# Performance work log

Measured on AMD Instinct MI355X. Metric: run time of the kernel, lower is better.

Reference implementation:

```python
import jax, jax.numpy as jnp
import numpy as np

N = 50000      # nodes
E = 600000     # edges (avg degree 12)
IN = 128       # in_feat
HID = IN // 2  # 64
OUT = 128      # out_feat (must equal in_feat, see msg_linear)

# NOTE: the torch source uses nn.LeakyReLU(True): the positional arg is
# negative_slope, so slope == 1.0 (identity). We reproduce that faithfully.
NEG_SLOPE = 1.0

def leaky(v):
    return jnp.where(v >= 0, v, NEG_SLOPE * v)

def _linear_params(key, fan_in, fan_out):
    kw, kb = jax.random.split(key)
    bound = 1.0 / np.sqrt(fan_in)
    W = jax.random.uniform(kw, (fan_in, fan_out), jnp.float32, -bound, bound)
    b = jax.random.uniform(kb, (fan_out,), jnp.float32, -bound, bound)
    return W, b

def setup_inputs() -> dict:
    key = jax.random.key(0)
    ks = jax.random.split(key, 10)
    x = jax.random.normal(ks[0], (N, IN), jnp.float32)
    e = jax.random.normal(ks[1], (E, IN), jnp.float32)
    src = jax.random.randint(ks[2], (E,), 0, N, jnp.int64)
    dst = jax.random.randint(ks[3], (E,), 0, N, jnp.int64)
    W_nl1, b_nl1 = _linear_params(ks[4], IN, HID)    # node_linear1
    W_el, b_el = _linear_params(ks[5], IN, HID)      # edge_linear
    W1, b1 = _linear_params(ks[6], HID, HID)         # node_mlp layer 1
    W2, b2 = _linear_params(ks[7], HID, OUT)         # node_mlp layer 2
    W_nl2, b_nl2 = _linear_params(ks[8], IN, HID)    # node_linear2
    km, ke = jax.random.split(ks[9])
    W_ml, b_ml = _linear_params(km, IN, HID)         # msg_linear (in_feat==out_feat)
    W_em, b_em = _linear_params(ke, HID, OUT)        # edge_mlp layer
    return dict(x=x, e=e, src=src, dst=dst,
                W_nl1=W_nl1, b_nl1=b_nl1, W_el=W_el, b_el=b_el,
                W1=W1, b1=b1, W2=W2, b2=b2,
                W_nl2=W_nl2, b_nl2=b_nl2, W_ml=W_ml, b_ml=b_ml,
                W_em=W_em, b_em=b_em)

def reference(x, e, src, dst,
              W_nl1, b_nl1, W_el, b_el,
              W1, b1, W2, b2,
              W_nl2, b_nl2, W_ml, b_ml,
              W_em, b_em):
    # apply_edges: e' = node_mlp(node_linear1(x[src]) + edge_linear(e))
    z = x[src] @ W_nl1 + b_nl1 + e @ W_el + b_el            # [E, HID]
    e_new = leaky(leaky(z) @ W1 + b1) @ W2 + b2             # [E, OUT]
    # update_all(copy_e, sum): scatter-sum edge messages to destination nodes
    msg = jax.ops.segment_sum(e_new, dst, num_segments=N)   # [N, OUT]
    # x' = edge_mlp(node_linear2(x) + msg_linear(msg))
    h = leaky(x @ W_nl2 + b_nl2 + msg @ W_ml + b_ml)        # [N, HID]
    return h @ W_em + b_em                                  # [N, OUT]
```

## Files before the change

kernel.cpp:

```cpp
#include <hip/hip_runtime.h>

#define N_NODES 50000
#define N_EDGES 600000

#define WF_XS   0
#define WF_ES   6400000
#define WF_UN   12800000
#define WI_CNT   16000000
#define WI_OFF   16050000
#define WI_CUR   16100000
#define WI_BSUM  16150000
#define WI_BOFF  16150256
#define WI_EPAIR 16150512
#define WF_T2   17350528
#define WF_BEG  17354624
#define WF_RH   17354752
#define WF_K1   17354816
#define WF_WA   17358912
#define WF_R    17383488
#define WF_C2   17383616

#define NBLK_SCAN 196

__global__ __launch_bounds__(256) void pre_t2_kernel(
        const float* __restrict__ W2, const float* __restrict__ W_ml,
        const float* __restrict__ b1, const float* __restrict__ b2,
        float* __restrict__ T2, float* __restrict__ be_g) {
    int idx = blockIdx.x * 256 + threadIdx.x;
    if (idx < 4096) {
        int i = idx >> 6, j = idx & 63;
        float s = 0.f;
        for (int k = 0; k < 128; ++k) s += W2[i*128+k] * W_ml[k*64+j];
        T2[idx] = s;
    } else if (idx < 4224) {
        int j = idx - 4096;
        float s = b2[j];
        for (int k = 0; k < 64; ++k) s += b1[k] * W2[k*128+j];
        be_g[j] = s;
    }
}

__global__ __launch_bounds__(256) void pre_k1_kernel(
        const float* __restrict__ W1, const float* __restrict__ T2,
        float* __restrict__ K1) {
    int idx = blockIdx.x * 256 + threadIdx.x;
    if (idx >= 4096) return;
    int i = idx >> 6, j = idx & 63;
    float s = 0.f;
    for (int k = 0; k < 64; ++k) s += W1[i*64+k] * T2[k*64+j];
    K1[idx] = s;
}

__global__ __launch_bounds__(256) void pre_wa_kernel(
        const float* __restrict__ W_nl1, const float* __restrict__ W_el,
        const float* __restrict__ W_nl2, const float* __restrict__ K1,
        const float* __restrict__ b_nl1, const float* __restrict__ b_el,
        const float* __restrict__ be_g, const float* __restrict__ W_ml,
        float* __restrict__ WA, float* __restrict__ rh_g) {
    int idx = blockIdx.x * 256 + threadIdx.x;
    if (idx < 8192) {
        WA[idx] = W_nl2[idx];
    } else if (idx < 16384) {
        int p = idx - 8192; int i = p >> 6, j = p & 63;
        float s = 0.f;
        for (int k = 0; k < 64; ++k) s += W_nl1[i*64+k] * K1[k*64+j];
        WA[idx] = s;
    } else if (idx < 24576) {
        int p = idx - 16384; int i = p >> 6, j = p & 63;
        float s = 0.f;
        for (int k = 0; k < 64; ++k) s += W_el[i*64+k] * K1[k*64+j];
        WA[idx] = s;
    } else if (idx < 24640) {
        int t = idx - 24576;
        float s = 0.f;
        for (int k = 0; k < 64; ++k)  s += (b_nl1[k] + b_el[k]) * K1[k*64+t];
        for (int k = 0; k < 128; ++k) s += be_g[k] * W_ml[k*64+t];
        rh_g[t] = s;
    }
}

__global__ __launch_bounds__(256) void pre_rc_kernel(
        const float* __restrict__ rh_g, const float* __restrict__ W_em,
        const float* __restrict__ b_nl2, const float* __restrict__ b_ml,
        const float* __restrict__ b_em,
        float* __restrict__ r, float* __restrict__ c2) {
    int idx = threadIdx.x;
    if (idx < 128) {
        float s = 0.f;
        for (int k = 0; k < 64; ++k) s += rh_g[k] * W_em[k*128+idx];
        r[idx] = s;
    } else {
        int j = idx - 128;
        float s = b_em[j];
        for (int k = 0; k < 64; ++k) s += (b_nl2[k] + b_ml[k]) * W_em[k*128+j];
        c2[j] = s;
    }
}

__global__ __launch_bounds__(256) void zero_kernel(int* __restrict__ cnt) {
    int i = blockIdx.x * 256 + threadIdx.x;
    if (i < N_NODES) cnt[i] = 0;
}

__global__ __launch_bounds__(256) void hist_kernel(const int* __restrict__ dst,
                                                   int* __restrict__ cnt) {
    int e = blockIdx.x * 256 + threadIdx.x;
    if (e < N_EDGES) atomicAdd(&cnt[dst[e]], 1);
}

__global__ __launch_bounds__(256) void scan_a_kernel(const int* __restrict__ cnt,
                                                     int* __restrict__ bsum) {
    __shared__ int s[256];
    int i = blockIdx.x * 256 + threadIdx.x;
    int v = (i < N_NODES) ? cnt[i] : 0;
    s[threadIdx.x] = v;
    __syncthreads();
    for (int d = 128; d > 0; d >>= 1) {
        if (threadIdx.x < d) s[threadIdx.x] += s[threadIdx.x + d];
        __syncthreads();
    }
    if (threadIdx.x == 0) bsum[blockIdx.x] = s[0];
}

__global__ __launch_bounds__(256) void scan_b_kernel(const int* __restrict__ bsum,
                                                     int* __restrict__ boff) {
    __shared__ int s[256];
    int t = threadIdx.x;
    int v = (t < NBLK_SCAN) ? bsum[t] : 0;
    s[t] = v;
    __syncthreads();
    for (int d = 1; d < 256; d <<= 1) {
        int tv = (t >= d) ? s[t - d] : 0;
        __syncthreads();
        s[t] += tv;
        __syncthreads();
    }
    if (t < NBLK_SCAN) boff[t] = s[t] - v;
}

__global__ __launch_bounds__(256) void scan_c_kernel(const int* __restrict__ cnt,
                                                     const int* __restrict__ boff,
                                                     int* __restrict__ offs,
                                                     int* __restrict__ cursor) {
    __shared__ int s[256];
    int i = blockIdx.x * 256 + threadIdx.x;
    int t = threadIdx.x;
    int v = (i < N_NODES) ? cnt[i] : 0;
    s[t] = v;
    __syncthreads();
    for (int d = 1; d < 256; d <<= 1) {
        int tv = (t >= d) ? s[t - d] : 0;
        __syncthreads();
        s[t] += tv;
        __syncthreads();
    }
    if (i < N_NODES) {
        int ex = s[t] - v + boff[blockIdx.x];
        offs[i] = ex;
        cursor[i] = ex;
    }
}

__global__ __launch_bounds__(256) void fill_kernel(const int* __restrict__ dst,
                                                   const int* __restrict__ src,
                                                   int* __restrict__ cursor,
                                                   int2* __restrict__ epair) {
    int e = blockIdx.x * 256 + threadIdx.x;
    if (e < N_EDGES) {
        int pos = atomicAdd(&cursor[dst[e]], 1);
        epair[pos] = make_int2(e, src[e]);
    }
}

__global__ __launch_bounds__(256) void gather_kernel(
        const float* __restrict__ x, const float* __restrict__ ef,
        const int* __restrict__ cnt, const int* __restrict__ offs,
        const int2* __restrict__ epair,
        float* __restrict__ xs, float* __restrict__ es) {
    int n    = (int)((blockIdx.x * 256 + threadIdx.x) >> 6);
    int lane = threadIdx.x & 63;
    if (n >= N_NODES) return;
    int off = offs[n], deg = cnt[n];
    int col2 = lane * 2;
    float ax0 = 0.f, ax1 = 0.f, ae0 = 0.f, ae1 = 0.f;
    for (int c0 = 0; c0 < deg; c0 += 64) {
        int j = c0 + lane;
        int2 p = make_int2(0, 0);
        if (j < deg) p = epair[off + j];
        int m = deg - c0; if (m > 64) m = 64;
        int j2 = 0;
        for (; j2 + 8 <= m; j2 += 8) {
            float2 xv[8], ev[8];
            #pragma unroll
            for (int u = 0; u < 8; ++u) {
                int e_ = __shfl(p.x, j2 + u);
                int s_ = __shfl(p.y, j2 + u);
                xv[u] = *(const float2*)(x  + (size_t)s_ * 128 + col2);
                ev[u] = *(const float2*)(ef + (size_t)e_ * 128 + col2);
            }
            #pragma unroll
            for (int u = 0; u < 8; ++u) {
                ax0 += xv[u].x; ax1 += xv[u].y;
                ae0 += ev[u].x; ae1 += ev[u].y;
            }
        }
        for (; j2 < m; ++j2) {
            int e_ = __shfl(p.x, j2);
            int s_ = __shfl(p.y, j2);
            float2 xv = *(const float2*)(x  + (size_t)s_ * 128 + col2);
            float2 ev = *(const float2*)(ef + (size_t)e_ * 128 + col2);
            ax0 += xv.x; ax1 += xv.y;
            ae0 += ev.x; ae1 += ev.y;
        }
    }
    *(float2*)(xs + (size_t)n * 128 + col2) = make_float2(ax0, ax1);
    *(float2*)(es + (size_t)n * 128 + col2) = make_float2(ae0, ae1);
}

__global__ __launch_bounds__(256) void gemm1_kernel(
        const float* __restrict__ x, const float* __restrict__ xs,
        const float* __restrict__ es, const float* __restrict__ WA,
        float* __restrict__ u) {
    __shared__ float As[32][133];
    __shared__ float Ws[32][64];
    int base = blockIdx.x * 128;
    int t = threadIdx.x;
    int cg = t & 15, rg = t >> 4;
    int c0 = cg * 4, r0 = rg * 8;

    float acc[8][4];
    #pragma unroll
    for (int i = 0; i < 8; ++i)
        #pragma unroll
        for (int j = 0; j < 4; ++j) acc[i][j] = 0.f;

    int arow0 = t >> 3;
    int akq   = t & 7;

    #pragma unroll
    for (int m = 0; m < 3; ++m) {
        const float* __restrict__ S = (m == 0) ? x : (m == 1) ? xs : es;
        for (int k0 = 0; k0 < 128; k0 += 32) {
            __syncthreads();
            #pragma unroll
            for (int i = 0; i < 4; ++i) {
                int row = arow0 + i * 32;
                int n = base + row;
                float4 v = make_float4(0.f, 0.f, 0.f, 0.f);
                if (n < N_NODES)
                    v = *(const float4*)&S[(size_t)n * 128 + k0 + akq * 4];
                As[akq * 4 + 0][row] = v.x;
                As[akq * 4 + 1][row] = v.y;
                As[akq * 4 + 2][row] = v.z;
                As[akq * 4 + 3][row] = v.w;
            }
            #pragma unroll
            for (int i = 0; i < 2; ++i) {
                int idx = t + i * 256;
                int row = idx >> 4, q4 = idx & 15;
                *(float4*)&Ws[row][q4 * 4] =
                    *(const float4*)&WA[(size_t)(m * 128 + k0 + row) * 64 + q4 * 4];
            }
            __syncthreads();
            #pragma unroll 8
            for (int k = 0; k < 32; ++k) {
                float a[8];
                *(float4*)&a[0] = *(const float4*)&As[k][r0];
                *(float4*)&a[4] = *(const float4*)&As[k][r0 + 4];
                float4 w = *(const float4*)&Ws[k][c0];
                #pragma unroll
                for (int i = 0; i < 8; ++i) {
                    acc[i][0] += a[i] * w.x;
                    acc[i][1] += a[i] * w.y;
                    acc[i][2] += a[i] * w.z;
                    acc[i][3] += a[i] * w.w;
                }
            }
        }
    }

    #pragma unroll
    for (int i = 0; i < 8; ++i) {
        int n = base + r0 + i;
        if (n < N_NODES)
            *(float4*)&u[(size_t)n * 64 + c0] = *(float4*)&acc[i][0];
    }
}

__global__ __launch_bounds__(256) void gemm2_kernel(
        const float* __restrict__ u, const int* __restrict__ cnt,
        const float* __restrict__ W_em,
        const float* __restrict__ rvec, const float* __restrict__ c2,
        float* __restrict__ out) {
    __shared__ float UsT[64][69];
    __shared__ float Wem[64][128];
    int base = blockIdx.x * 64;
    int t = threadIdx.x;
    int cg = t & 15, rg = t >> 4;
    int c0 = cg * 8, r0 = rg * 4;

    #pragma unroll
    for (int i = 0; i < 4; ++i) {
        int idx = t + i * 256;
        int row = idx >> 4, kq = idx & 15;
        int n = base + row;
        float4 v = make_float4(0.f, 0.f, 0.f, 0.f);
        if (n < N_NODES) v = *(const float4*)&u[(size_t)n * 64 + kq * 4];
        UsT[kq * 4 + 0][row] = v.x;
        UsT[kq * 4 + 1][row] = v.y;
        UsT[kq * 4 + 2][row] = v.z;
        UsT[kq * 4 + 3][row] = v.w;
    }
    #pragma unroll
    for (int i = 0; i < 8; ++i) {
        int idx = t + i * 256;
        int row = idx >> 5, q4 = idx & 31;
        *(float4*)&Wem[row][q4 * 4] = *(const float4*)&W_em[(size_t)row * 128 + q4 * 4];
    }

    float4 rva = *(const float4*)&rvec[c0];
    float4 rvb = *(const float4*)&rvec[c0 + 4];
    float4 cva = *(const float4*)&c2[c0];
    float4 cvb = *(const float4*)&c2[c0 + 4];
    float acc[4][8];
    #pragma unroll
    for (int i = 0; i < 4; ++i) {
        int n = base + r0 + i;
        float dg = (n < N_NODES) ? (float)cnt[n] : 0.f;
        acc[i][0] = cva.x + dg * rva.x;  acc[i][1] = cva.y + dg * rva.y;
        acc[i][2] = cva.z + dg * rva.z;  acc[i][3] = cva.w + dg * rva.w;
        acc[i][4] = cvb.x + dg * rvb.x;  acc[i][5] = cvb.y + dg * rvb.y;
        acc[i][6] = cvb.z + dg * rvb.z;  acc[i][7] = cvb.w + dg * rvb.w;
    }
    __syncthreads();

    #pragma unroll 8
    for (int k = 0; k < 64; ++k) {
        float a[4], w[8];
        *(float4*)&a[0] = *(const float4*)&UsT[k][r0];
        *(float4*)&w[0] = *(const float4*)&Wem[k][c0];
        *(float4*)&w[4] = *(const float4*)&Wem[k][c0 + 4];
        #pragma unroll
        for (int i = 0; i < 4; ++i)
            #pragma unroll
            for (int j = 0; j < 8; ++j)
                acc[i][j] += a[i] * w[j];
    }

    #pragma unroll
    for (int i = 0; i < 4; ++i) {
        int n = base + r0 + i;
        if (n < N_NODES) {
            *(float4*)&out[(size_t)n * 128 + c0]     = *(float4*)&acc[i][0];
            *(float4*)&out[(size_t)n * 128 + c0 + 4] = *(float4*)&acc[i][4];
        }
    }
}

extern "C" void kernel_launch(void* const* d_in, const int* in_sizes, int n_in,
                              void* d_out, int out_size, void* d_ws, size_t ws_size,
                              hipStream_t stream) {
    const float* x     = (const float*)d_in[0];
    const float* ef    = (const float*)d_in[1];
    const int*   src   = (const int*)d_in[2];
    const int*   dst   = (const int*)d_in[3];
    const float* W_nl1 = (const float*)d_in[4];
    const float* b_nl1 = (const float*)d_in[5];
    const float* W_el  = (const float*)d_in[6];
    const float* b_el  = (const float*)d_in[7];
    const float* W1    = (const float*)d_in[8];
    const float* b1    = (const float*)d_in[9];
    const float* W2    = (const float*)d_in[10];
    const float* b2    = (const float*)d_in[11];
    const float* W_nl2 = (const float*)d_in[12];
    const float* b_nl2 = (const float*)d_in[13];
    const float* W_ml  = (const float*)d_in[14];
    const float* b_ml  = (const float*)d_in[15];
    const float* W_em  = (const float*)d_in[16];
    const float* b_em  = (const float*)d_in[17];

    int*   wsI = (int*)d_ws;
    float* wsF = (float*)d_ws;
    float* xs     = wsF + WF_XS;
    float* es     = wsF + WF_ES;
    float* uN     = wsF + WF_UN;
    int*   cnt    = wsI + WI_CNT;
    int*   offs   = wsI + WI_OFF;
    int*   cursor = wsI + WI_CUR;
    int*   bsum   = wsI + WI_BSUM;
    int*   boff   = wsI + WI_BOFF;
    int2*  epair  = (int2*)(wsI + WI_EPAIR);
    float* T2   = wsF + WF_T2;
    float* be_g = wsF + WF_BEG;
    float* rh_g = wsF + WF_RH;
    float* K1   = wsF + WF_K1;
    float* WA   = wsF + WF_WA;
    float* r    = wsF + WF_R;
    float* c2   = wsF + WF_C2;

    pre_t2_kernel<<<17, 256, 0, stream>>>(W2, W_ml, b1, b2, T2, be_g);
    pre_k1_kernel<<<16, 256, 0, stream>>>(W1, T2, K1);
    pre_wa_kernel<<<97, 256, 0, stream>>>(W_nl1, W_el, W_nl2, K1,
                                          b_nl1, b_el, be_g, W_ml, WA, rh_g);
    pre_rc_kernel<<<1, 256, 0, stream>>>(rh_g, W_em, b_nl2, b_ml, b_em, r, c2);

    zero_kernel<<<NBLK_SCAN, 256, 0, stream>>>(cnt);
    hist_kernel<<<(N_EDGES + 255) / 256, 256, 0, stream>>>(dst, cnt);
    scan_a_kernel<<<NBLK_SCAN, 256, 0, stream>>>(cnt, bsum);
    scan_b_kernel<<<1, 256, 0, stream>>>(bsum, boff);
    scan_c_kernel<<<NBLK_SCAN, 256, 0, stream>>>(cnt, boff, offs, cursor);
    fill_kernel<<<(N_EDGES + 255) / 256, 256, 0, stream>>>(dst, src, cursor, epair);

    gather_kernel<<<(N_NODES + 3) / 4, 256, 0, stream>>>(
        x, ef, cnt, offs, epair, xs, es);

    gemm1_kernel<<<(N_NODES + 127) / 128, 256, 0, stream>>>(x, xs, es, WA, uN);
    gemm2_kernel<<<(N_NODES + 63) / 64, 256, 0, stream>>>(
        uN, cnt, W_em, r, c2, (float*)d_out);
}
```

Measured before the change: 278.9 us.

## Project x to 64-dim before gathering to halve gathered node feature traffic

```diff
diff --git a/kernel.cpp b/kernel.cpp
--- a/kernel.cpp
+++ b/kernel.cpp
@@ -3,8 +3,11 @@
 #define N_NODES 50000
 #define N_EDGES 600000
 
-#define WF_XS   0
-#define WF_ES   6400000
+typedef float v2f __attribute__((ext_vector_type(2)));
+
+#define WF_PX   0
+#define WF_ES   3200000
+#define WF_PXS  9600000
 #define WF_UN   12800000
 #define WI_CNT   16000000
 #define WI_OFF   16050000
@@ -17,6 +20,7 @@
 #define WF_RH   17354752
 #define WF_K1   17354816
 #define WF_WA   17358912
+#define WF_WX1  17375296
 #define WF_R    17383488
 #define WF_C2   17383616
 
@@ -56,20 +60,21 @@
         const float* __restrict__ W_nl2, const float* __restrict__ K1,
         const float* __restrict__ b_nl1, const float* __restrict__ b_el,
         const float* __restrict__ be_g, const float* __restrict__ W_ml,
-        float* __restrict__ WA, float* __restrict__ rh_g) {
+        float* __restrict__ WA, float* __restrict__ WX1,
+        float* __restrict__ rh_g) {
     int idx = blockIdx.x * 256 + threadIdx.x;
     if (idx < 8192) {
         WA[idx] = W_nl2[idx];
     } else if (idx < 16384) {
         int p = idx - 8192; int i = p >> 6, j = p & 63;
         float s = 0.f;
-        for (int k = 0; k < 64; ++k) s += W_nl1[i*64+k] * K1[k*64+j];
+        for (int k = 0; k < 64; ++k) s += W_el[i*64+k] * K1[k*64+j];
         WA[idx] = s;
     } else if (idx < 24576) {
         int p = idx - 16384; int i = p >> 6, j = p & 63;
         float s = 0.f;
-        for (int k = 0; k < 64; ++k) s += W_el[i*64+k] * K1[k*64+j];
-        WA[idx] = s;
+        for (int k = 0; k < 64; ++k) s += W_nl1[i*64+k] * K1[k*64+j];
+        WX1[p] = s;
     } else if (idx < 24640) {
         int t = idx - 24576;
         float s = 0.f;
@@ -172,54 +177,115 @@
     }
 }
 
+__global__ __launch_bounds__(256) void px_kernel(
+        const float* __restrict__ x, const float* __restrict__ WX1,
+        float* __restrict__ px) {
+    __shared__ float As[32][133];
+    __shared__ float Ws[32][64];
+    int base = blockIdx.x * 128;
+    int t = threadIdx.x;
+    int cg = t & 15, rg = t >> 4;
+    int c0 = cg * 4, r0 = rg * 8;
+
+    float acc[8][4];
+    #pragma unroll
+    for (int i = 0; i < 8; ++i)
+        #pragma unroll
+        for (int j = 0; j < 4; ++j) acc[i][j] = 0.f;
+
+    int arow0 = t >> 3;
+    int akq   = t & 7;
+
+    for (int k0 = 0; k0 < 128; k0 += 32) {
+        __syncthreads();
+        #pragma unroll
+        for (int i = 0; i < 4; ++i) {
+            int row = arow0 + i * 32;
+            int n = base + row;
+            float4 v = make_float4(0.f, 0.f, 0.f, 0.f);
+            if (n < N_NODES)
+                v = *(const float4*)&x[(size_t)n * 128 + k0 + akq * 4];
+            As[akq * 4 + 0][row] = v.x;
+            As[akq * 4 + 1][row] = v.y;
+            As[akq * 4 + 2][row] = v.z;
+            As[akq * 4 + 3][row] = v.w;
+        }
+        #pragma unroll
+        for (int i = 0; i < 2; ++i) {
+            int idx = t + i * 256;
+            int row = idx >> 4, q4 = idx & 15;
+            *(float4*)&Ws[row][q4 * 4] =
+                *(const float4*)&WX1[(size_t)(k0 + row) * 64 + q4 * 4];
+        }
+        __syncthreads();
+        #pragma unroll 8
+        for (int k = 0; k < 32; ++k) {
+            float a[8];
+            *(float4*)&a[0] = *(const float4*)&As[k][r0];
+            *(float4*)&a[4] = *(const float4*)&As[k][r0 + 4];
+            float4 w = *(const float4*)&Ws[k][c0];
+            #pragma unroll
+            for (int i = 0; i < 8; ++i) {
+                acc[i][0] += a[i] * w.x;
+                acc[i][1] += a[i] * w.y;
+                acc[i][2] += a[i] * w.z;
+                acc[i][3] += a[i] * w.w;
+            }
+        }
+    }
+
+    #pragma unroll
+    for (int i = 0; i < 8; ++i) {
+        int n = base + r0 + i;
+        if (n < N_NODES)
+            *(float4*)&px[(size_t)n * 64 + c0] = *(float4*)&acc[i][0];
+    }
+}
+
 __global__ __launch_bounds__(256) void gather_kernel(
-        const float* __restrict__ x, const float* __restrict__ ef,
+        const float* __restrict__ px, const float* __restrict__ ef,
         const int* __restrict__ cnt, const int* __restrict__ offs,
         const int2* __restrict__ epair,
-        float* __restrict__ xs, float* __restrict__ es) {
+        float* __restrict__ pxs, float* __restrict__ es) {
     int n    = (int)((blockIdx.x * 256 + threadIdx.x) >> 6);
     int lane = threadIdx.x & 63;
     if (n >= N_NODES) return;
     int off = offs[n], deg = cnt[n];
     int col2 = lane * 2;
-    float ax0 = 0.f, ax1 = 0.f, ae0 = 0.f, ae1 = 0.f;
+    float apx = 0.f, ae0 = 0.f, ae1 = 0.f;
     for (int c0 = 0; c0 < deg; c0 += 64) {
         int j = c0 + lane;
         int2 p = make_int2(0, 0);
         if (j < deg) p = epair[off + j];
         int m = deg - c0; if (m > 64) m = 64;
-        int j2 = 0;
-        for (; j2 + 8 <= m; j2 += 8) {
-            float2 xv[8], ev[8];
+        for (int j2 = 0; j2 < m; j2 += 8) {
+            float xv[8]; v2f ev[8]; float msk[8];
             #pragma unroll
             for (int u = 0; u < 8; ++u) {
-                int e_ = __shfl(p.x, j2 + u);
-                int s_ = __shfl(p.y, j2 + u);
-                xv[u] = *(const float2*)(x  + (size_t)s_ * 128 + col2);
-                ev[u] = *(const float2*)(ef + (size_t)e_ * 128 + col2);
+                int jj = j2 + u;
+                int idx = (jj < m) ? jj : (m - 1);
+                msk[u] = (jj < m) ? 1.f : 0.f;
+                int e_ = __shfl(p.x, idx);
+                int s_ = __shfl(p.y, idx);
+                xv[u] = px[(size_t)s_ * 64 + lane];
+                ev[u] = __builtin_nontemporal_load(
+                            (const v2f*)(ef + (size_t)e_ * 128 + col2));
             }
             #pragma unroll
             for (int u = 0; u < 8; ++u) {
-                ax0 += xv[u].x; ax1 += xv[u].y;
-                ae0 += ev[u].x; ae1 += ev[u].y;
-            }
-        }
-        for (; j2 < m; ++j2) {
-            int e_ = __shfl(p.x, j2);
-            int s_ = __shfl(p.y, j2);
-            float2 xv = *(const float2*)(x  + (size_t)s_ * 128 + col2);
-            float2 ev = *(const float2*)(ef + (size_t)e_ * 128 + col2);
-            ax0 += xv.x; ax1 += xv.y;
-            ae0 += ev.x; ae1 += ev.y;
-        }
-    }
-    *(float2*)(xs + (size_t)n * 128 + col2) = make_float2(ax0, ax1);
+                apx += msk[u] * xv[u];
+                ae0 += msk[u] * ev[u][0];
+                ae1 += msk[u] * ev[u][1];
+            }
+        }
+    }
+    pxs[(size_t)n * 64 + lane] = apx;
     *(float2*)(es + (size_t)n * 128 + col2) = make_float2(ae0, ae1);
 }
 
 __global__ __launch_bounds__(256) void gemm1_kernel(
-        const float* __restrict__ x, const float* __restrict__ xs,
-        const float* __restrict__ es, const float* __restrict__ WA,
+        const float* __restrict__ x, const float* __restrict__ es,
+        const float* __restrict__ pxs, const float* __restrict__ WA,
         float* __restrict__ u) {
     __shared__ float As[32][133];
     __shared__ float Ws[32][64];
@@ -230,16 +296,19 @@
 
     float acc[8][4];
     #pragma unroll
-    for (int i = 0; i < 8; ++i)
-        #pragma unroll
-        for (int j = 0; j < 4; ++j) acc[i][j] = 0.f;
+    for (int i = 0; i < 8; ++i) {
+        int n = base + r0 + i;
+        float4 pv = make_float4(0.f, 0.f, 0.f, 0.f);
+        if (n < N_NODES) pv = *(const float4*)&pxs[(size_t)n * 64 + c0];
+        acc[i][0] = pv.x; acc[i][1] = pv.y; acc[i][2] = pv.z; acc[i][3] = pv.w;
+    }
 
     int arow0 = t >> 3;
     int akq   = t & 7;
 
     #pragma unroll
-    for (int m = 0; m < 3; ++m) {
-        const float* __restrict__ S = (m == 0) ? x : (m == 1) ? xs : es;
+    for (int m = 0; m < 2; ++m) {
+        const float* __restrict__ S = (m == 0) ? x : es;
         for (int k0 = 0; k0 < 128; k0 += 32) {
             __syncthreads();
             #pragma unroll
@@ -381,8 +450,9 @@
 
     int*   wsI = (int*)d_ws;
     float* wsF = (float*)d_ws;
-    float* xs     = wsF + WF_XS;
+    float* px     = wsF + WF_PX;
     float* es     = wsF + WF_ES;
+    float* pxs    = wsF + WF_PXS;
     float* uN     = wsF + WF_UN;
     int*   cnt    = wsI + WI_CNT;
     int*   offs   = wsI + WI_OFF;
@@ -395,13 +465,14 @@
     float* rh_g = wsF + WF_RH;
     float* K1   = wsF + WF_K1;
     float* WA   = wsF + WF_WA;
+    float* WX1  = wsF + WF_WX1;
     float* r    = wsF + WF_R;
     float* c2   = wsF + WF_C2;
 
     pre_t2_kernel<<<17, 256, 0, stream>>>(W2, W_ml, b1, b2, T2, be_g);
     pre_k1_kernel<<<16, 256, 0, stream>>>(W1, T2, K1);
     pre_wa_kernel<<<97, 256, 0, stream>>>(W_nl1, W_el, W_nl2, K1,
-                                          b_nl1, b_el, be_g, W_ml, WA, rh_g);
+                                          b_nl1, b_el, be_g, W_ml, WA, WX1, rh_g);
     pre_rc_kernel<<<1, 256, 0, stream>>>(rh_g, W_em, b_nl2, b_ml, b_em, r, c2);
 
     zero_kernel<<<NBLK_SCAN, 256, 0, stream>>>(cnt);
@@ -411,10 +482,12 @@
     scan_c_kernel<<<NBLK_SCAN, 256, 0, stream>>>(cnt, boff, offs, cursor);
     fill_kernel<<<(N_EDGES + 255) / 256, 256, 0, stream>>>(dst, src, cursor, epair);
 
+    px_kernel<<<(N_NODES + 127) / 128, 256, 0, stream>>>(x, WX1, px);
+
     gather_kernel<<<(N_NODES + 3) / 4, 256, 0, stream>>>(
-        x, ef, cnt, offs, epair, xs, es);
-
-    gemm1_kernel<<<(N_NODES + 127) / 128, 256, 0, stream>>>(x, xs, es, WA, uN);
+        px, ef, cnt, offs, epair, pxs, es);
+
+    gemm1_kernel<<<(N_NODES + 127) / 128, 256, 0, stream>>>(x, es, pxs, WA, uN);
     gemm2_kernel<<<(N_NODES + 63) / 64, 256, 0, stream>>>(
         uN, cnt, W_em, r, c2, (float*)d_out);
 }
```

Measured after the change: 252.2 us. -9.6%, faster.

## Precompute node projections before gather and fuse small setup kernels

Applied to the files above, without the earlier changes.

```diff
diff --git a/kernel.cpp b/kernel.cpp
--- a/kernel.cpp
+++ b/kernel.cpp
@@ -3,139 +3,152 @@
 #define N_NODES 50000
 #define N_EDGES 600000
 
-#define WF_XS   0
-#define WF_ES   6400000
-#define WF_UN   12800000
-#define WI_CNT   16000000
-#define WI_OFF   16050000
-#define WI_CUR   16100000
-#define WI_BSUM  16150000
-#define WI_BOFF  16150256
-#define WI_EPAIR 16150512
-#define WF_T2   17350528
-#define WF_BEG  17354624
-#define WF_RH   17354752
-#define WF_K1   17354816
-#define WF_WA   17358912
-#define WF_R    17383488
-#define WF_C2   17383616
+typedef float v2f __attribute__((ext_vector_type(2)));
+
+#define WF_PA   0
+#define WF_UN   6400000
+#define WI_CNT   9600000
+#define WI_OFF   9650000
+#define WI_CUR   9700000
+#define WI_BSUM  9750000
+#define WI_BOFF  9750256
+#define WI_EPAIR 9750512
+#define WF_T2   10950528
+#define WF_BEG  10954624
+#define WF_RH   10954752
+#define WF_K1   10954816
+#define WF_WAX  10958912
+#define WF_WE   10975296
+#define WF_R    10983488
+#define WF_C2   10983616
 
 #define NBLK_SCAN 196
-
-__global__ __launch_bounds__(256) void pre_t2_kernel(
+#define NBLK_E    2344
+#define NBLK_PT2  17
+#define NBLK_K1   16
+#define NBLK_WA   97
+#define NBLK_PXA  391
+
+__global__ __launch_bounds__(256) void f1_pret2_zero(
         const float* __restrict__ W2, const float* __restrict__ W_ml,
         const float* __restrict__ b1, const float* __restrict__ b2,
-        float* __restrict__ T2, float* __restrict__ be_g) {
-    int idx = blockIdx.x * 256 + threadIdx.x;
-    if (idx < 4096) {
+        float* __restrict__ T2, float* __restrict__ be_g,
+        int* __restrict__ cnt) {
+    int bid = blockIdx.x;
+    if (bid < NBLK_PT2) {
+        int idx = bid * 256 + threadIdx.x;
+        if (idx < 4096) {
+            int i = idx >> 6, j = idx & 63;
+            float s = 0.f;
+            for (int k = 0; k < 128; ++k) s += W2[i*128+k] * W_ml[k*64+j];
+            T2[idx] = s;
+        } else if (idx < 4224) {
+            int j = idx - 4096;
+            float s = b2[j];
+            for (int k = 0; k < 64; ++k) s += b1[k] * W2[k*128+j];
+            be_g[j] = s;
+        }
+    } else {
+        int i = (bid - NBLK_PT2) * 256 + threadIdx.x;
+        if (i < N_NODES) cnt[i] = 0;
+    }
+}
+
+__global__ __launch_bounds__(256) void f2_prek1_hist(
+        const float* __restrict__ W1, const float* __restrict__ T2,
+        float* __restrict__ K1,
+        const int* __restrict__ dst, int* __restrict__ cnt) {
+    int bid = blockIdx.x;
+    if (bid < NBLK_K1) {
+        int idx = bid * 256 + threadIdx.x;
         int i = idx >> 6, j = idx & 63;
         float s = 0.f;
-        for (int k = 0; k < 128; ++k) s += W2[i*128+k] * W_ml[k*64+j];
-        T2[idx] = s;
-    } else if (idx < 4224) {
-        int j = idx - 4096;
-        float s = b2[j];
-        for (int k = 0; k < 64; ++k) s += b1[k] * W2[k*128+j];
-        be_g[j] = s;
-    }
-}
-
-__global__ __launch_bounds__(256) void pre_k1_kernel(
-        const float* __restrict__ W1, const float* __restrict__ T2,
-        float* __restrict__ K1) {
-    int idx = blockIdx.x * 256 + threadIdx.x;
-    if (idx >= 4096) return;
-    int i = idx >> 6, j = idx & 63;
-    float s = 0.f;
-    for (int k = 0; k < 64; ++k) s += W1[i*64+k] * T2[k*64+j];
-    K1[idx] = s;
-}
-
-__global__ __launch_bounds__(256) void pre_wa_kernel(
+        for (int k = 0; k < 64; ++k) s += W1[i*64+k] * T2[k*64+j];
+        K1[idx] = s;
+    } else {
+        int e = (bid - NBLK_K1) * 256 + threadIdx.x;
+        if (e < N_EDGES) atomicAdd(&cnt[dst[e]], 1);
+    }
+}
+
+__global__ __launch_bounds__(256) void f3_prewa_scana(
         const float* __restrict__ W_nl1, const float* __restrict__ W_el,
         const float* __restrict__ W_nl2, const float* __restrict__ K1,
         const float* __restrict__ b_nl1, const float* __restrict__ b_el,
         const float* __restrict__ be_g, const float* __restrict__ W_ml,
-        float* __restrict__ WA, float* __restrict__ rh_g) {
-    int idx = blockIdx.x * 256 + threadIdx.x;
-    if (idx < 8192) {
-        WA[idx] = W_nl2[idx];
-    } else if (idx < 16384) {
-        int p = idx - 8192; int i = p >> 6, j = p & 63;
-        float s = 0.f;
-        for (int k = 0; k < 64; ++k) s += W_nl1[i*64+k] * K1[k*64+j];
-        WA[idx] = s;
-    } else if (idx < 24576) {
-        int p = idx - 16384; int i = p >> 6, j = p & 63;
-        float s = 0.f;
-        for (int k = 0; k < 64; ++k) s += W_el[i*64+k] * K1[k*64+j];
-        WA[idx] = s;
-    } else if (idx < 24640) {
-        int t = idx - 24576;
-        float s = 0.f;
-        for (int k = 0; k < 64; ++k)  s += (b_nl1[k] + b_el[k]) * K1[k*64+t];
-        for (int k = 0; k < 128; ++k) s += be_g[k] * W_ml[k*64+t];
-        rh_g[t] = s;
-    }
-}
-
-__global__ __launch_bounds__(256) void pre_rc_kernel(
+        float* __restrict__ WAX, float* __restrict__ WE,
+        float* __restrict__ rh_g,
+        const int* __restrict__ cnt, int* __restrict__ bsum) {
+    int bid = blockIdx.x;
+    if (bid < NBLK_WA) {
+        int idx = bid * 256 + threadIdx.x;
+        if (idx < 16384) {
+            int i = idx >> 7, j = idx & 127;
+            if (j < 64) {
+                WAX[idx] = W_nl2[i*64+j];
+            } else {
+                float s = 0.f;
+                for (int k = 0; k < 64; ++k) s += W_nl1[i*64+k] * K1[k*64+(j-64)];
+                WAX[idx] = s;
+            }
+        } else if (idx < 24576) {
+            int p = idx - 16384; int i = p >> 6, j = p & 63;
+            float s = 0.f;
+            for (int k = 0; k < 64; ++k) s += W_el[i*64+k] * K1[k*64+j];
+            WE[p] = s;
+        } else if (idx < 24640) {
+            int t = idx - 24576;
+            float s = 0.f;
+            for (int k = 0; k < 64; ++k)  s += (b_nl1[k] + b_el[k]) * K1[k*64+t];
+            for (int k = 0; k < 128; ++k) s += be_g[k] * W_ml[k*64+t];
+            rh_g[t] = s;
+        }
+    } else {
+        __shared__ int s[256];
+        int blk = bid - NBLK_WA;
+        int i = blk * 256 + threadIdx.x;
+        int v = (i < N_NODES) ? cnt[i] : 0;
+        s[threadIdx.x] = v;
+        __syncthreads();
+        for (int d = 128; d > 0; d >>= 1) {
+            if (threadIdx.x < d) s[threadIdx.x] += s[threadIdx.x + d];
+            __syncthreads();
+        }
+        if (threadIdx.x == 0) bsum[blk] = s[0];
+    }
+}
+
+__global__ __launch_bounds__(256) void f4_prerc_scanb(
         const float* __restrict__ rh_g, const float* __restrict__ W_em,
         const float* __restrict__ b_nl2, const float* __restrict__ b_ml,
         const float* __restrict__ b_em,
-        float* __restrict__ r, float* __restrict__ c2) {
-    int idx = threadIdx.x;
-    if (idx < 128) {
-        float s = 0.f;
-        for (int k = 0; k < 64; ++k) s += rh_g[k] * W_em[k*128+idx];
-        r[idx] = s;
+        float* __restrict__ r, float* __restrict__ c2,
+        const int* __restrict__ bsum, int* __restrict__ boff) {
+    int t = threadIdx.x;
+    if (blockIdx.x == 0) {
+        if (t < 128) {
+            float s = 0.f;
+            for (int k = 0; k < 64; ++k) s += rh_g[k] * W_em[k*128+t];
+            r[t] = s;
+        } else {
+            int j = t - 128;
+            float s = b_em[j];
+            for (int k = 0; k < 64; ++k) s += (b_nl2[k] + b_ml[k]) * W_em[k*128+j];
+            c2[j] = s;
+        }
     } else {
-        int j = idx - 128;
-        float s = b_em[j];
-        for (int k = 0; k < 64; ++k) s += (b_nl2[k] + b_ml[k]) * W_em[k*128+j];
-        c2[j] = s;
-    }
-}
-
-__global__ __launch_bounds__(256) void zero_kernel(int* __restrict__ cnt) {
-    int i = blockIdx.x * 256 + threadIdx.x;
-    if (i < N_NODES) cnt[i] = 0;
-}
-
-__global__ __launch_bounds__(256) void hist_kernel(const int* __restrict__ dst,
-                                                   int* __restrict__ cnt) {
-    int e = blockIdx.x * 256 + threadIdx.x;
-    if (e < N_EDGES) atomicAdd(&cnt[dst[e]], 1);
-}
-
-__global__ __launch_bounds__(256) void scan_a_kernel(const int* __restrict__ cnt,
-                                                     int* __restrict__ bsum) {
-    __shared__ int s[256];
-    int i = blockIdx.x * 256 + threadIdx.x;
-    int v = (i < N_NODES) ? cnt[i] : 0;
-    s[threadIdx.x] = v;
-    __syncthreads();
-    for (int d = 128; d > 0; d >>= 1) {
-        if (threadIdx.x < d) s[threadIdx.x] += s[threadIdx.x + d];
-        __syncthreads();
-    }
-    if (threadIdx.x == 0) bsum[blockIdx.x] = s[0];
-}
-
-__global__ __launch_bounds__(256) void scan_b_kernel(const int* __restrict__ bsum,
-                                                     int* __restrict__ boff) {
-    __shared__ int s[256];
-    int t = threadIdx.x;
-    int v = (t < NBLK_SCAN) ? bsum[t] : 0;
-    s[t] = v;
-    __syncthreads();
-    for (int d = 1; d < 256; d <<= 1) {
-        int tv = (t >= d) ? s[t - d] : 0;
-        __syncthreads();
-        s[t] += tv;
-        __syncthreads();
-    }
-    if (t < NBLK_SCAN) boff[t] = s[t] - v;
+        __shared__ int s[256];
+        int v = (t < NBLK_SCAN) ? bsum[t] : 0;
+        s[t] = v;
+        __syncthreads();
+        for (int d = 1; d < 256; d <<= 1) {
+            int tv = (t >= d) ? s[t - d] : 0;
+            __syncthreads();
+            s[t] += tv;
+            __syncthreads();
+        }
+        if (t < NBLK_SCAN) boff[t] = s[t] - v;
+    }
 }
 
 __global__ __launch_bounds__(256) void scan_c_kernel(const int* __restrict__ cnt,
@@ -161,130 +174,137 @@
     }
 }
 
-__global__ __launch_bounds__(256) void fill_kernel(const int* __restrict__ dst,
-                                                   const int* __restrict__ src,
-                                                   int* __restrict__ cursor,
-                                                   int2* __restrict__ epair) {
-    int e = blockIdx.x * 256 + threadIdx.x;
-    if (e < N_EDGES) {
-        int pos = atomicAdd(&cursor[dst[e]], 1);
-        epair[pos] = make_int2(e, src[e]);
+__global__ __launch_bounds__(256) void f5_fill_pxa(
+        const int* __restrict__ dst, const int* __restrict__ src,
+        int* __restrict__ cursor, int2* __restrict__ epair,
+        const float* __restrict__ x, const float* __restrict__ WAX,
+        float* __restrict__ PA) {
+    int bid = blockIdx.x;
+    if (bid < NBLK_E) {
+        int e = bid * 256 + threadIdx.x;
+        if (e < N_EDGES) {
+            int pos = atomicAdd(&cursor[dst[e]], 1);
+            epair[pos] = make_int2(e, src[e]);
+        }
+        return;
+    }
+    __shared__ float As[32][133];
+    __shared__ float Ws[32][128];
+    int base = (bid - NBLK_E) * 128;
+    int t = threadIdx.x;
+    int cg = t & 15, rg = t >> 4;
+    int c0 = cg * 8, r0 = rg * 8;
+
+    float acc[8][8];
+    #pragma unroll
+    for (int i = 0; i < 8; ++i)
+        #pragma unroll
+        for (int j = 0; j < 8; ++j) acc[i][j] = 0.f;
+
+    int arow0 = t >> 3;
+    int akq   = t & 7;
+
+    for (int k0 = 0; k0 < 128; k0 += 32) {
+        __syncthreads();
+        #pragma unroll
+        for (int i = 0; i < 4; ++i) {
+            int row = arow0 + i * 32;
+            int n = base + row;
+            float4 v = make_float4(0.f, 0.f, 0.f, 0.f);
+            if (n < N_NODES)
+                v = *(const float4*)&x[(size_t)n * 128 + k0 + akq * 4];
+            As[akq * 4 + 0][row] = v.x;
+            As[akq * 4 + 1][row] = v.y;
+            As[akq * 4 + 2][row] = v.z;
+            As[akq * 4 + 3][row] = v.w;
+        }
+        #pragma unroll
+        for (int i = 0; i < 4; ++i) {
+            int idx = t + i * 256;
+            int row = idx >> 5, q4 = idx & 31;
+            *(float4*)&Ws[row][q4 * 4] =
+                *(const float4*)&WAX[(size_t)(k0 + row) * 128 + q4 * 4];
+        }
+        __syncthreads();
+        #pragma unroll 8
+        for (int k = 0; k < 32; ++k) {
+            float a[8], w[8];
+            *(float4*)&a[0] = *(const float4*)&As[k][r0];
+            *(float4*)&a[4] = *(const float4*)&As[k][r0 + 4];
+            *(float4*)&w[0] = *(const float4*)&Ws[k][c0];
+            *(float4*)&w[4] = *(const float4*)&Ws[k][c0 + 4];
+            #pragma unroll
+            for (int i = 0; i < 8; ++i)
+                #pragma unroll
+                for (int jj = 0; jj < 8; ++jj)
+                    acc[i][jj] += a[i] * w[jj];
+        }
+    }
+
+    #pragma unroll
+    for (int i = 0; i < 8; ++i) {
+        int n = base + r0 + i;
+        if (n < N_NODES) {
+            *(float4*)&PA[(size_t)n * 128 + c0]     = *(float4*)&acc[i][0];
+            *(float4*)&PA[(size_t)n * 128 + c0 + 4] = *(float4*)&acc[i][4];
+        }
     }
 }
 
 __global__ __launch_bounds__(256) void gather_kernel(
-        const float* __restrict__ x, const float* __restrict__ ef,
+        const float* __restrict__ PA, const float* __restrict__ ef,
         const int* __restrict__ cnt, const int* __restrict__ offs,
-        const int2* __restrict__ epair,
-        float* __restrict__ xs, float* __restrict__ es) {
+        const int2* __restrict__ epair, const float* __restrict__ WE,
+        float* __restrict__ u) {
     int n    = (int)((blockIdx.x * 256 + threadIdx.x) >> 6);
     int lane = threadIdx.x & 63;
     if (n >= N_NODES) return;
     int off = offs[n], deg = cnt[n];
     int col2 = lane * 2;
-    float ax0 = 0.f, ax1 = 0.f, ae0 = 0.f, ae1 = 0.f;
+    float a_val = PA[(size_t)n * 128 + lane];
+    float apx = 0.f, ae0 = 0.f, ae1 = 0.f;
     for (int c0 = 0; c0 < deg; c0 += 64) {
         int j = c0 + lane;
         int2 p = make_int2(0, 0);
         if (j < deg) p = epair[off + j];
         int m = deg - c0; if (m > 64) m = 64;
-        int j2 = 0;
-        for (; j2 + 8 <= m; j2 += 8) {
-            float2 xv[8], ev[8];
+        for (int j2 = 0; j2 < m; j2 += 8) {
+            float xv[8]; v2f ev[8]; float msk[8];
             #pragma unroll
-            for (int u = 0; u < 8; ++u) {
-                int e_ = __shfl(p.x, j2 + u);
-                int s_ = __shfl(p.y, j2 + u);
-                xv[u] = *(const float2*)(x  + (size_t)s_ * 128 + col2);
-                ev[u] = *(const float2*)(ef + (size_t)e_ * 128 + col2);
+            for (int uu = 0; uu < 8; ++uu) {
+                int jj = j2 + uu;
+                int idx = (jj < m) ? jj : (m - 1);
+                msk[uu] = (jj < m) ? 1.f : 0.f;
+                int e_ = __shfl(p.x, idx);
+                int s_ = __shfl(p.y, idx);
+                xv[uu] = PA[(size_t)s_ * 128 + 64 + lane];
+                ev[uu] = __builtin_nontemporal_load(
+                            (const v2f*)(ef + (size_t)e_ * 128 + col2));
             }
             #pragma unroll
-            for (int u = 0; u < 8; ++u) {
-                ax0 += xv[u].x; ax1 += xv[u].y;
-                ae0 += ev[u].x; ae1 += ev[u].y;
+            for (int uu = 0; uu < 8; ++uu) {
+                apx += msk[uu] * xv[uu];
+                ae0 += msk[uu] * ev[uu][0];
+                ae1 += msk[uu] * ev[uu][1];
             }
         }
-        for (; j2 < m; ++j2) {
-            int e_ = __shfl(p.x, j2);
-            int s_ = __shfl(p.y, j2);
-            float2 xv = *(const float2*)(x  + (size_t)s_ * 128 + col2);
-            float2 ev = *(const float2*)(ef + (size_t)e_ * 128 + col2);
-            ax0 += xv.x; ax1 += xv.y;
-            ae0 += ev.x; ae1 += ev.y;
-        }
-    }
-    *(float2*)(xs + (size_t)n * 128 + col2) = make_float2(ax0, ax1);
-    *(float2*)(es + (size_t)n * 128 + col2) = make_float2(ae0, ae1);
-}
-
-__global__ __launch_bounds__(256) void gemm1_kernel(
-        const float* __restrict__ x, const float* __restrict__ xs,
-        const float* __restrict__ es, const float* __restrict__ WA,
-        float* __restrict__ u) {
-    __shared__ float As[32][133];
-    __shared__ float Ws[32][64];
-    int base = blockIdx.x * 128;
-    int t = threadIdx.x;
-    int cg = t & 15, rg = t >> 4;
-    int c0 = cg * 4, r0 = rg * 8;
-
-    float acc[8][4];
-    #pragma unroll
-    for (int i = 0; i < 8; ++i)
+    }
+    const float* WEl = WE + lane;
+    float pr0 = 0.f, pr1 = 0.f, pr2 = 0.f, pr3 = 0.f;
+    for (int k0 = 0; k0 < 128; k0 += 8) {
+        float wv[8], evv[8];
         #pragma unroll
-        for (int j = 0; j < 4; ++j) acc[i][j] = 0.f;
-
-    int arow0 = t >> 3;
-    int akq   = t & 7;
-
-    #pragma unroll
-    for (int m = 0; m < 3; ++m) {
-        const float* __restrict__ S = (m == 0) ? x : (m == 1) ? xs : es;
-        for (int k0 = 0; k0 < 128; k0 += 32) {
-            __syncthreads();
-            #pragma unroll
-            for (int i = 0; i < 4; ++i) {
-                int row = arow0 + i * 32;
-                int n = base + row;
-                float4 v = make_float4(0.f, 0.f, 0.f, 0.f);
-                if (n < N_NODES)
-                    v = *(const float4*)&S[(size_t)n * 128 + k0 + akq * 4];
-                As[akq * 4 + 0][row] = v.x;
-                As[akq * 4 + 1][row] = v.y;
-                As[akq * 4 + 2][row] = v.z;
-                As[akq * 4 + 3][row] = v.w;
-            }
-            #pragma unroll
-            for (int i = 0; i < 2; ++i) {
-                int idx = t + i * 256;
-                int row = idx >> 4, q4 = idx & 15;
-                *(float4*)&Ws[row][q4 * 4] =
-                    *(const float4*)&WA[(size_t)(m * 128 + k0 + row) * 64 + q4 * 4];
-            }
-            __syncthreads();
-            #pragma unroll 8
-            for (int k = 0; k < 32; ++k) {
-                float a[8];
-                *(float4*)&a[0] = *(const float4*)&As[k][r0];
-                *(float4*)&a[4] = *(const float4*)&As[k][r0 + 4];
-                float4 w = *(const float4*)&Ws[k][c0];
-                #pragma unroll
-                for (int i = 0; i < 8; ++i) {
-                    acc[i][0] += a[i] * w.x;
-                    acc[i][1] += a[i] * w.y;
-                    acc[i][2] += a[i] * w.z;
-                    acc[i][3] += a[i] * w.w;
-                }
-            }
-        }
-    }
-
-    #pragma unroll
-    for (int i = 0; i < 8; ++i) {
-        int n = base + r0 + i;
-        if (n < N_NODES)
-            *(float4*)&u[(size_t)n * 64 + c0] = *(float4*)&acc[i][0];
-    }
+        for (int uu = 0; uu < 8; ++uu) {
+            int kk = k0 + uu;
+            wv[uu]  = WEl[kk * 64];
+            evv[uu] = __shfl((kk & 1) ? ae1 : ae0, kk >> 1);
+        }
+        pr0 += evv[0]*wv[0] + evv[4]*wv[4];
+        pr1 += evv[1]*wv[1] + evv[5]*wv[5];
+        pr2 += evv[2]*wv[2] + evv[6]*wv[6];
+        pr3 += evv[3]*wv[3] + evv[7]*wv[7];
+    }
+    u[(size_t)n * 64 + lane] = a_val + apx + ((pr0 + pr1) + (pr2 + pr3));
 }
 
 __global__ __launch_bounds__(256) void gemm2_kernel(
@@ -381,8 +401,7 @@
 
     int*   wsI = (int*)d_ws;
     float* wsF = (float*)d_ws;
-    float* xs     = wsF + WF_XS;
-    float* es     = wsF + WF_ES;
+    float* PA     = wsF + WF_PA;
     float* uN     = wsF + WF_UN;
     int*   cnt    = wsI + WI_CNT;
     int*   offs   = wsI + WI_OFF;
@@ -394,27 +413,27 @@
     float* be_g = wsF + WF_BEG;
     float* rh_g = wsF + WF_RH;
     float* K1   = wsF + WF_K1;
-    float* WA   = wsF + WF_WA;
+    float* WAX  = wsF + WF_WAX;
+    float* WE   = wsF + WF_WE;
     float* r    = wsF + WF_R;
     float* c2   = wsF + WF_C2;
 
-    pre_t2_kernel<<<17, 256, 0, stream>>>(W2, W_ml, b1, b2, T2, be_g);
-    pre_k1_kernel<<<16, 256, 0, stream>>>(W1, T2, K1);
-    pre_wa_kernel<<<97, 256, 0, stream>>>(W_nl1, W_el, W_nl2, K1,
-                                          b_nl1, b_el, be_g, W_ml, WA, rh_g);
-    pre_rc_kernel<<<1, 256, 0, stream>>>(rh_g, W_em, b_nl2, b_ml, b_em, r, c2);
-
-    zero_kernel<<<NBLK_SCAN, 256, 0, stream>>>(cnt);
-    hist_kernel<<<(N_EDGES + 255) / 256, 256, 0, stream>>>(dst, cnt);
-    scan_a_kernel<<<NBLK_SCAN, 256, 0, stream>>>(cnt, bsum);
-    scan_b_kernel<<<1, 256, 0, stream>>>(bsum, boff);
+    f1_pret2_zero<<<NBLK_PT2 + NBLK_SCAN, 256, 0, stream>>>(
+        W2, W_ml, b1, b2, T2, be_g, cnt);
+    f2_prek1_hist<<<NBLK_K1 + NBLK_E, 256, 0, stream>>>(
+        W1, T2, K1, dst, cnt);
+    f3_prewa_scana<<<NBLK_WA + NBLK_SCAN, 256, 0, stream>>>(
+        W_nl1, W_el, W_nl2, K1, b_nl1, b_el, be_g, W_ml, WAX, WE, rh_g,
+        cnt, bsum);
+    f4_prerc_scanb<<<2, 256, 0, stream>>>(
+        rh_g, W_em, b_nl2, b_ml, b_em, r, c2, bsum, boff);
     scan_c_kernel<<<NBLK_SCAN, 256, 0, stream>>>(cnt, boff, offs, cursor);
-    fill_kernel<<<(N_EDGES + 255) / 256, 256, 0, stream>>>(dst, src, cursor, epair);
+    f5_fill_pxa<<<NBLK_E + NBLK_PXA, 256, 0, stream>>>(
+        dst, src, cursor, epair, x, WAX, PA);
 
     gather_kernel<<<(N_NODES + 3) / 4, 256, 0, stream>>>(
-        x, ef, cnt, offs, epair, xs, es);
-
-    gemm1_kernel<<<(N_NODES + 127) / 128, 256, 0, stream>>>(x, xs, es, WA, uN);
+        PA, ef, cnt, offs, epair, WE, uN);
+
     gemm2_kernel<<<(N_NODES + 63) / 64, 256, 0, stream>>>(
         uN, cnt, W_em, r, c2, (float*)d_out);
 }
```

New measurement: 281.6 us. No clear change (+1.0%).
